# Kernel tuning notes

Measured on AMD Instinct MI355X. Metric: run time of the kernel, lower is better.

## Reference

```python
import jax, jax.numpy as jnp
import numpy as np

DIM = 192
HEADS = 4
CTX = 256
HID = int(DIM * 2.66)  # 510


def _dwconv(x, w):
    # x: (b,c,h,w), w: (c,1,3,3) depthwise
    return jax.lax.conv_general_dilated(
        x, w, window_strides=(1, 1), padding='SAME',
        dimension_numbers=('NCHW', 'OIHW', 'NCHW'),
        feature_group_count=x.shape[1])


def _conv1x1(x, w):
    # w: (out, in)
    return jnp.einsum('oc,bchw->bohw', w, x)


def _layernorm(x, weight, bias):
    # WithBias LayerNorm over channel dim (last dim after to_3d == channels)
    mu = x.mean(axis=1, keepdims=True)
    var = ((x - mu) ** 2).mean(axis=1, keepdims=True)
    xn = (x - mu) / jnp.sqrt(var + 1e-5)
    return xn * weight[None, :, None, None] + bias[None, :, None, None]


def setup_inputs() -> dict:
    key = jax.random.key(0)
    ks = jax.random.split(key, 16)
    s = 0.02
    inp = {
        'x': jax.random.normal(ks[0], (8, DIM, 128, 128), jnp.float32),
        'context_emb': jax.random.normal(ks[1], (8, CTX), jnp.float32),
        'ln1_w': jnp.ones((DIM,), jnp.float32),
        'ln1_b': jnp.zeros((DIM,), jnp.float32),
        'ln2_w': jnp.ones((DIM,), jnp.float32),
        'ln2_b': jnp.zeros((DIM,), jnp.float32),
        'w_qkv': jax.random.normal(ks[2], (3 * DIM, DIM), jnp.float32) * s,
        'w_qkv_dw': jax.random.normal(ks[3], (3 * DIM, 1, 3, 3), jnp.float32) * s,
        'w_proj': jax.random.normal(ks[4], (DIM, DIM), jnp.float32) * s,
        'base_temp': jnp.ones((HEADS, 1, 1), jnp.float32),
        'ta_w1': jax.random.normal(ks[5], (DIM // 4, CTX), jnp.float32) * s,
        'ta_b1': jnp.zeros((DIM // 4,), jnp.float32),
        'ta_w2': jax.random.normal(ks[6], (HEADS, DIM // 4), jnp.float32) * s,
        'ta_b2': jnp.zeros((HEADS,), jnp.float32),
        'vg_w': jax.random.normal(ks[7], (DIM, CTX), jnp.float32) * s,
        'vg_b': jnp.zeros((DIM,), jnp.float32),
        'w_local': jax.random.normal(ks[8], (DIM, 1, 3, 3), jnp.float32) * s,
        'w_ffn_in': jax.random.normal(ks[9], (2 * HID, DIM), jnp.float32) * s,
        'w_ffn_dw': jax.random.normal(ks[10], (2 * HID, 1, 3, 3), jnp.float32) * s,
        'w_ffn_out': jax.random.normal(ks[11], (DIM, HID), jnp.float32) * s,
    }
    return inp


def _forward(x, context_emb, ln1_w, ln1_b, ln2_w, ln2_b, w_qkv, w_qkv_dw,
             w_proj, base_temp, ta_w1, ta_b1, ta_w2, ta_b2, vg_w, vg_b,
             w_local, w_ffn_in, w_ffn_dw, w_ffn_out):
    b, c, h, w = x.shape
    hd = c // HEADS
    scale = hd ** (-0.5)

    # ---- Attention branch ----
    residual = x
    xn = _layernorm(x, ln1_w, ln1_b)

    # context adapters
    t = jax.nn.relu(context_emb @ ta_w1.T + ta_b1) @ ta_w2.T + ta_b2  # (b,heads)
    temp_factor = jax.nn.sigmoid(t)[:, :, None, None] * 2.0 + 0.5    # (b,heads,1,1)
    total_temp = base_temp[None] * temp_factor
    v_gate = jax.nn.sigmoid(context_emb @ vg_w.T + vg_b)             # (b,dim)
    v_gate = v_gate.reshape(b, HEADS, hd, 1)

    qkv = _dwconv(_conv1x1(xn, w_qkv), w_qkv_dw)
    q, k, v = jnp.split(qkv, 3, axis=1)

    def heads_flat(t4):
        return t4.reshape(b, HEADS, hd, h * w)

    qf = heads_flat(q)
    kf = heads_flat(k)
    vf = heads_flat(v)
    qf = qf / jnp.maximum(jnp.linalg.norm(qf, axis=-1, keepdims=True), 1e-12)
    kf = kf / jnp.maximum(jnp.linalg.norm(kf, axis=-1, keepdims=True), 1e-12)

    attn = jnp.einsum('bhcn,bhdn->bhcd', qf, kf) * scale  # (b,heads,hd,hd)
    attn = jax.nn.softmax(attn * total_temp, axis=-1)

    out_global = jnp.einsum('bhcd,bhdn->bhcn', attn, vf * v_gate)
    out_global = out_global.reshape(b, c, h, w)
    out_local = _dwconv(v, w_local)
    x = residual + _conv1x1(out_global + out_local, w_proj)

    # ---- GDFN branch ----
    residual = x
    xn = _layernorm(x, ln2_w, ln2_b)
    y = _dwconv(_conv1x1(xn, w_ffn_in), w_ffn_dw)
    y1, y2 = jnp.split(y, 2, axis=1)
    y = jax.nn.gelu(y1, approximate=False) * y2
    x = residual + _conv1x1(y, w_ffn_out)
    return x


def reference(x, context_emb, ln1_w, ln1_b, ln2_w, ln2_b, w_qkv, w_qkv_dw,
              w_proj, base_temp, ta_w1, ta_b1, ta_w2, ta_b2, vg_w, vg_b,
              w_local, w_ffn_in, w_ffn_dw, w_ffn_out):
    return _forward(x, context_emb, ln1_w, ln1_b, ln2_w, ln2_b, w_qkv,
                    w_qkv_dw, w_proj, base_temp, ta_w1, ta_b1, ta_w2, ta_b2,
                    vg_w, vg_b, w_local, w_ffn_in, w_ffn_dw, w_ffn_out)
```

## Files before the change

### kernel.cpp

```cpp
#include <hip/hip_runtime.h>
#include <math.h>

#define NB 8
#define NC 192
#define NH 128
#define NW 128
#define HW 16384
#define NQ 576
#define NHID 510
#define NHIDP 512
#define NG2 1020
#define NG2P 1024

#define BROWS 32
#define BSLOTS 34
#define BPIX (BSLOTS * NW)
#define BIPIX (BROWS * NW)

typedef unsigned short u16;
typedef short s16x8 __attribute__((ext_vector_type(8)));
typedef float f32x4 __attribute__((ext_vector_type(4)));

#define MFMA_BF16(a, b, c) __builtin_amdgcn_mfma_f32_16x16x32_bf16((a), (b), (c), 0, 0, 0)

__device__ __forceinline__ u16 f2bf(float f) {
  union { float f; unsigned u; } v; v.f = f;
  unsigned r = v.u + 0x7fffu + ((v.u >> 16) & 1u);
  return (u16)(r >> 16);
}
__device__ __forceinline__ float bf2f(u16 h) {
  union { unsigned u; float f; } v; v.u = ((unsigned)h) << 16; return v.f;
}
__device__ __forceinline__ float lo2f(unsigned u) {
  union { unsigned u; float f; } v; v.u = u << 16; return v.f;
}
__device__ __forceinline__ float hi2f(unsigned u) {
  union { unsigned u; float f; } v; v.u = u & 0xffff0000u; return v.f;
}

__global__ void k_prep(const float* __restrict__ wq, const float* __restrict__ wfi,
                       const float* __restrict__ wfo,
                       u16* __restrict__ oq, u16* __restrict__ ofi, u16* __restrict__ ofo) {
  const int n1 = NQ * NC, n2 = NG2P * NC, n3 = NC * NHIDP;
  for (int i = blockIdx.x * blockDim.x + threadIdx.x; i < n1 + n2 + n3;
       i += gridDim.x * blockDim.x) {
    if (i < n1) {
      oq[i] = f2bf(wq[i]);
    } else if (i < n1 + n2) {
      int j = i - n1; int row = j / NC;
      u16 v = 0;
      if (row < NG2) v = f2bf(wfi[j]);
      ofi[j] = v;
    } else {
      int j = i - n1 - n2; int row = j >> 9, col = j & 511;
      u16 v = 0;
      if (col < NHID) v = f2bf(wfo[row * NHID + col]);
      ofo[j] = v;
    }
  }
}

__global__ void k_ctx(const float* __restrict__ ce, const float* __restrict__ taw1,
                      const float* __restrict__ tab1, const float* __restrict__ taw2,
                      const float* __restrict__ tab2, const float* __restrict__ vgw,
                      const float* __restrict__ vgb, const float* __restrict__ btemp,
                      float* __restrict__ tempt, float* __restrict__ vg) {
  int b = blockIdx.x, t = threadIdx.x;
  __shared__ float sce[256];
  __shared__ float shid[48];
  sce[t] = ce[b * 256 + t];
  __syncthreads();
  if (t < 48) {
    float s = tab1[t];
    for (int j = 0; j < 256; j++) s = fmaf(taw1[t * 256 + j], sce[j], s);
    shid[t] = fmaxf(s, 0.f);
  }
  __syncthreads();
  if (t < 4) {
    float s = tab2[t];
    for (int j = 0; j < 48; j++) s = fmaf(taw2[t * 48 + j], shid[j], s);
    float sg = 1.f / (1.f + expf(-s));
    tempt[b * 4 + t] = btemp[t] * (sg * 2.f + 0.5f);
  }
  if (t < 192) {
    float s = vgb[t];
    for (int j = 0; j < 256; j++) s = fmaf(vgw[t * 256 + j], sce[j], s);
    vg[b * 192 + t] = 1.f / (1.f + expf(-s));
  }
}

__global__ __launch_bounds__(256, 2)
void k_ln_gemm_band(const float* __restrict__ in, const float* __restrict__ lnw,
                    const float* __restrict__ lnb, const u16* __restrict__ wbf,
                    u16* __restrict__ out, int nchunks, int row_start, int slot0) {
  __shared__ u16 Xn[64 * 200];
  __shared__ u16 Wc[64 * 200];
  __shared__ float red[512];
  __shared__ float stats[128];
  int t = threadIdx.x;
  int lane = t & 63, wv = t >> 6;
  int bpb = gridDim.x >> 3;
  int b = blockIdx.x / bpb;
  int rb = blockIdx.x - b * bpb;
  int gpx0 = row_start * NW + rb * 64;
  int opx0 = slot0 * NW + rb * 64;
  const float* xp = in + (size_t)b * NC * HW + gpx0 + lane;
  float vals[48];
  float s = 0.f, s2 = 0.f;
#pragma unroll
  for (int j = 0; j < 48; j++) {
    float v = xp[(size_t)(wv * 48 + j) * HW];
    vals[j] = v; s += v; s2 = fmaf(v, v, s2);
  }
  red[wv * 64 + lane] = s;
  red[256 + wv * 64 + lane] = s2;
  __syncthreads();
  if (t < 64) {
    float m = 0.f, q = 0.f;
#pragma unroll
    for (int k = 0; k < 4; k++) { m += red[k * 64 + t]; q += red[256 + k * 64 + t]; }
    m *= (1.f / 192.f);
    float var = q * (1.f / 192.f) - m * m;
    stats[t] = m; stats[64 + t] = rsqrtf(var + 1e-5f);
  }
  __syncthreads();
  float mu = stats[lane], rs = stats[64 + lane];
#pragma unroll
  for (int j = 0; j < 48; j += 2) {
    int c = wv * 48 + j;
    float xa = (vals[j] - mu) * rs * lnw[c] + lnb[c];
    float xb = (vals[j + 1] - mu) * rs * lnw[c + 1] + lnb[c + 1];
    *(unsigned*)&Xn[lane * 200 + c] = (unsigned)f2bf(xa) | ((unsigned)f2bf(xb) << 16);
  }
  int r = lane & 15, grp = lane >> 4;
  int ostride = nchunks << 6;
  for (int nc = 0; nc < nchunks; nc++) {
    __syncthreads();
    for (int i = t; i < 1536; i += 256) {
      int row = i / 24, sg = i % 24;
      *(s16x8*)&Wc[row * 200 + sg * 8] =
          *(const s16x8*)&wbf[(size_t)(nc * 64 + row) * 192 + sg * 8];
    }
    __syncthreads();
    f32x4 z = {0.f, 0.f, 0.f, 0.f};
    f32x4 acc0 = z, acc1 = z, acc2 = z, acc3 = z;
#pragma unroll
    for (int ks = 0; ks < 6; ks++) {
      int k0 = ks * 32 + grp * 8;
      s16x8 a = *(s16x8*)&Xn[(wv * 16 + r) * 200 + k0];
      acc0 = MFMA_BF16(a, *(s16x8*)&Wc[r * 200 + k0], acc0);
      acc1 = MFMA_BF16(a, *(s16x8*)&Wc[(16 + r) * 200 + k0], acc1);
      acc2 = MFMA_BF16(a, *(s16x8*)&Wc[(32 + r) * 200 + k0], acc2);
      acc3 = MFMA_BF16(a, *(s16x8*)&Wc[(48 + r) * 200 + k0], acc3);
    }
    u16* op = out + ((size_t)b * BPIX + opx0 + wv * 16 + grp * 4) * ostride + nc * 64 + r;
#pragma unroll
    for (int i = 0; i < 4; i++) {
      op[(size_t)i * ostride] = f2bf(acc0[i]);
      op[(size_t)i * ostride + 16] = f2bf(acc1[i]);
      op[(size_t)i * ostride + 32] = f2bf(acc2[i]);
      op[(size_t)i * ostride + 48] = f2bf(acc3[i]);
    }
  }
}

__global__ __launch_bounds__(256, 4)
void k_dw_attn_band(const u16* __restrict__ qb_band, const float* __restrict__ wdw,
                    u16* __restrict__ qkb, u16* __restrict__ vpm,
                    float* __restrict__ ssq, int r0) {
  __shared__ u16 Hl[6 * 18 * 64];
  __shared__ float sred[8 * 64];
  int t = threadIdx.x;
  int cc = blockIdx.x % 9;
  int rem = blockIdx.x / 9;
  int b = rem >> 6; int r2 = rem & 63;
  int h0l = (r2 >> 3) * 4, w0 = (r2 & 7) * 16;
  int c0 = cc * 64;
  const s16x8 z8 = {0, 0, 0, 0, 0, 0, 0, 0};
  for (int i = t; i < 864; i += 256) {
    int px = i >> 3, sg = i & 7;
    int hh = px / 18, ww = px % 18;
    int slot = h0l + hh;
    int gh = r0 - 1 + slot;
    int gw = w0 - 1 + ww;
    s16x8 v = z8;
    if (gh >= 0 && gh < NH && gw >= 0 && gw < NW)
      v = *(const s16x8*)&qb_band[((size_t)b * BPIX + slot * NW + gw) * NQ + c0 + sg * 8];
    *(s16x8*)&Hl[(hh * 18 + ww) * 64 + sg * 8] = v;
  }
  __syncthreads();
  int cp = t & 31, psub = t >> 5;
  int pr = psub >> 1, pc0 = (psub & 1) * 8;
  int gc = c0 + 2 * cp;
  float wg0[9], wg1[9];
#pragma unroll
  for (int q = 0; q < 9; q++) { wg0[q] = wdw[gc * 9 + q]; wg1[q] = wdw[(gc + 1) * 9 + q]; }
  bool isv = (c0 >= 384);
  float sq0 = 0.f, sq1 = 0.f;
  s16x8 ov0 = z8, ov1 = z8;
#pragma unroll
  for (int j = 0; j < 8; j++) {
    int pc = pc0 + j;
    float a0 = 0.f, a1 = 0.f;
#pragma unroll
    for (int dr = 0; dr < 3; dr++)
#pragma unroll
      for (int dc = 0; dc < 3; dc++) {
        unsigned u = *(const unsigned*)&Hl[((pr + dr) * 18 + pc + dc) * 64 + 2 * cp];
        a0 = fmaf(lo2f(u), wg0[dr * 3 + dc], a0);
        a1 = fmaf(hi2f(u), wg1[dr * 3 + dc], a1);
      }
    u16 u0 = f2bf(a0), u1 = f2bf(a1);
    if (isv) {
      int gp = (r0 + h0l + pr) * NW + w0 + pc;
      *(unsigned*)&vpm[((size_t)b * HW + gp) * 192 + (gc - 384)] =
          (unsigned)u0 | ((unsigned)u1 << 16);
    } else {
      ov0[j] = (short)u0; ov1[j] = (short)u1;
      float f0 = bf2f(u0), f1 = bf2f(u1);
      sq0 = fmaf(f0, f0, sq0); sq1 = fmaf(f1, f1, sq1);
    }
  }
  if (!isv) {
    int lpx = (h0l + pr) * NW + w0 + pc0;
    *(s16x8*)&qkb[((size_t)b * 384 + gc) * BIPIX + lpx] = ov0;
    *(s16x8*)&qkb[((size_t)b * 384 + gc + 1) * BIPIX + lpx] = ov1;
    sred[psub * 64 + 2 * cp] = sq0;
    sred[psub * 64 + 2 * cp + 1] = sq1;
    __syncthreads();
    if (t < 64) {
      float sa = 0.f;
#pragma unroll
      for (int p8 = 0; p8 < 8; p8++) sa += sred[p8 * 64 + t];
      atomicAdd(&ssq[b * 384 + c0 + t], sa);
    }
  }
}

__global__ __launch_bounds__(256, 2)
void k_attn_band(const u16* __restrict__ qkb, float* __restrict__ attn) {
  __shared__ float par[4 * 2304];
  int t = threadIdx.x;
  int lane = t & 63, wv = t >> 6;
  int r = lane & 15, grp = lane >> 4;
  int bh = blockIdx.x >> 2, kc = blockIdx.x & 3;
  int b = bh >> 2, h = bh & 3;
  const u16* qb = qkb + ((size_t)b * 384 + h * 48) * BIPIX;
  const u16* kb = qkb + ((size_t)b * 384 + 192 + h * 48) * BIPIX;
  f32x4 z = {0.f, 0.f, 0.f, 0.f};
  f32x4 acc[3][3];
#pragma unroll
  for (int i = 0; i < 3; i++)
#pragma unroll
    for (int j = 0; j < 3; j++) acc[i][j] = z;
  int kbase = kc * 1024 + wv * 256 + grp * 8;
#pragma unroll 2
  for (int ks = 0; ks < 8; ks++) {
    int k0 = kbase + ks * 32;
    s16x8 af[3], bf[3];
#pragma unroll
    for (int mt = 0; mt < 3; mt++) af[mt] = *(const s16x8*)&qb[(size_t)(mt * 16 + r) * BIPIX + k0];
#pragma unroll
    for (int nt = 0; nt < 3; nt++) bf[nt] = *(const s16x8*)&kb[(size_t)(nt * 16 + r) * BIPIX + k0];
#pragma unroll
    for (int mt = 0; mt < 3; mt++)
#pragma unroll
      for (int nt = 0; nt < 3; nt++) acc[mt][nt] = MFMA_BF16(af[mt], bf[nt], acc[mt][nt]);
  }
#pragma unroll
  for (int mt = 0; mt < 3; mt++)
#pragma unroll
    for (int nt = 0; nt < 3; nt++)
#pragma unroll
      for (int i = 0; i < 4; i++)
        par[wv * 2304 + (mt * 16 + grp * 4 + i) * 48 + nt * 16 + r] = acc[mt][nt][i];
  __syncthreads();
  float* ag = attn + (size_t)bh * 2304;
  for (int i = t; i < 2304; i += 256)
    atomicAdd(&ag[i], par[i] + par[2304 + i] + par[4608 + i] + par[6912 + i]);
}

__global__ void k_softmax(float* __restrict__ attn, const float* __restrict__ ssq,
                          const float* __restrict__ tempt, const float* __restrict__ vg) {
  int bh = blockIdx.x, b = bh >> 2, h = bh & 3;
  int t = threadIdx.x;
  __shared__ float srk[48], svg[48];
  if (t < 48) {
    float nk = sqrtf(ssq[b * 384 + 192 + h * 48 + t]);
    srk[t] = 1.f / fmaxf(nk, 1e-12f);
    svg[t] = vg[b * 192 + h * 48 + t];
  }
  __syncthreads();
  if (t < 48) {
    float nq = sqrtf(ssq[b * 384 + h * 48 + t]);
    float rq = 1.f / fmaxf(nq, 1e-12f);
    float sc = 0.14433756729740643f * tempt[b * 4 + h] * rq;
    float* row = attn + (size_t)bh * 2304 + t * 48;
    float l[48]; float mx = -1e30f;
#pragma unroll
    for (int d = 0; d < 48; d++) { l[d] = row[d] * srk[d] * sc; mx = fmaxf(mx, l[d]); }
    float ss = 0.f;
#pragma unroll
    for (int d = 0; d < 48; d++) { l[d] = expf(l[d] - mx); ss += l[d]; }
    float inv = 1.f / ss;
#pragma unroll
    for (int d = 0; d < 48; d++) row[d] = l[d] * inv * svg[d];
  }
}

__global__ __launch_bounds__(256)
void k_wd(const float* __restrict__ attn, const float* __restrict__ wp,
          u16* __restrict__ wdg) {
  __shared__ float am[4 * 48 * 48];
  int b = blockIdx.x >> 3, oc = blockIdx.x & 7;
  int t = threadIdx.x;
  const float* ag = attn + (size_t)b * 4 * 2304;
  for (int i = t; i < 9216; i += 256) am[i] = ag[i];
  __syncthreads();
  u16* wdb = wdg + (size_t)b * 192 * 384;
  for (int idx = t; idx < 24 * 384; idx += 256) {
    int oo = idx / 384, j = idx % 384;
    int o = oc * 24 + oo;
    float val;
    if (j < 192) {
      int hj = j / 48, dj = j % 48;
      const float* wpo = wp + o * 192 + hj * 48;
      const float* ap = am + hj * 2304 + dj;
      float sa = 0.f;
#pragma unroll
      for (int c = 0; c < 48; c++) sa = fmaf(wpo[c], ap[c * 48], sa);
      val = sa;
    } else {
      val = wp[o * 192 + (j - 192)];
    }
    wdb[o * 384 + j] = f2bf(val);
  }
}

__global__ __launch_bounds__(256, 2)
void k_proj(const u16* __restrict__ vpm, const float* __restrict__ wl,
            const u16* __restrict__ wdg, const float* __restrict__ x,
            float* __restrict__ x2) {
  __shared__ u16 Hl[6 * 18 * 64];
  __shared__ u16 Xl[64 * 392];
  int t = threadIdx.x;
  int b = blockIdx.x >> 8; int r2 = blockIdx.x & 255;
  int h0 = (r2 >> 3) * 4, w0 = (r2 & 7) * 16;
  int cp = t & 31, psub = t >> 5;
  int pr = psub >> 1, pc0 = (psub & 1) * 8;
  const s16x8 z8 = {0, 0, 0, 0, 0, 0, 0, 0};
  for (int c3 = 0; c3 < 3; c3++) {
    int c0 = c3 * 64;
    __syncthreads();
    for (int i = t; i < 864; i += 256) {
      int px = i >> 3, sg = i & 7;
      int hh = px / 18, ww = px % 18;
      int gh = h0 - 1 + hh, gw = w0 - 1 + ww;
      s16x8 v = z8;
      if (gh >= 0 && gh < NH && gw >= 0 && gw < NW)
        v = *(const s16x8*)&vpm[((size_t)b * HW + gh * NW + gw) * 192 + c0 + sg * 8];
      *(s16x8*)&Hl[(hh * 18 + ww) * 64 + sg * 8] = v;
    }
    __syncthreads();
    int gc = c0 + 2 * cp;
    float wg0[9], wg1[9];
#pragma unroll
    for (int q = 0; q < 9; q++) { wg0[q] = wl[gc * 9 + q]; wg1[q] = wl[(gc + 1) * 9 + q]; }
#pragma unroll
    for (int j = 0; j < 8; j++) {
      int pc = pc0 + j; int p = pr * 16 + pc;
      float a0 = 0.f, a1 = 0.f; unsigned uc = 0;
#pragma unroll
      for (int dr = 0; dr < 3; dr++)
#pragma unroll
        for (int dc = 0; dc < 3; dc++) {
          unsigned u = *(const unsigned*)&Hl[((pr + dr) * 18 + pc + dc) * 64 + 2 * cp];
          if (dr == 1 && dc == 1) uc = u;
          a0 = fmaf(lo2f(u), wg0[dr * 3 + dc], a0);
          a1 = fmaf(hi2f(u), wg1[dr * 3 + dc], a1);
        }
      *(unsigned*)&Xl[p * 392 + gc] = uc;
      *(unsigned*)&Xl[p * 392 + 192 + gc] =
          (unsigned)f2bf(a0) | ((unsigned)f2bf(a1) << 16);
    }
  }
  __syncthreads();
  int lane = t & 63, wv = t >> 6;
  int r = lane & 15, grp = lane >> 4;
  const u16* wdb = wdg + (size_t)b * 192 * 384;
  f32x4 z = {0.f, 0.f, 0.f, 0.f};
  f32x4 acc[3][4];
#pragma unroll
  for (int i = 0; i < 3; i++)
#pragma unroll
    for (int j = 0; j < 4; j++) acc[i][j] = z;
#pragma unroll 2
  for (int ks = 0; ks < 12; ks++) {
    int k0 = ks * 32 + grp * 8;
    s16x8 b0 = *(s16x8*)&Xl[r * 392 + k0];
    s16x8 b1 = *(s16x8*)&Xl[(16 + r) * 392 + k0];
    s16x8 b2 = *(s16x8*)&Xl[(32 + r) * 392 + k0];
    s16x8 b3 = *(s16x8*)&Xl[(48 + r) * 392 + k0];
#pragma unroll
    for (int mt = 0; mt < 3; mt++) {
      s16x8 a = *(const s16x8*)&wdb[(size_t)(wv * 48 + mt * 16 + r) * 384 + k0];
      acc[mt][0] = MFMA_BF16(a, b0, acc[mt][0]);
      acc[mt][1] = MFMA_BF16(a, b1, acc[mt][1]);
      acc[mt][2] = MFMA_BF16(a, b2, acc[mt][2]);
      acc[mt][3] = MFMA_BF16(a, b3, acc[mt][3]);
    }
  }
#pragma unroll
  for (int mt = 0; mt < 3; mt++)
#pragma unroll
    for (int nt = 0; nt < 4; nt++) {
      size_t base = ((size_t)b * NC + wv * 48 + mt * 16 + grp * 4) * HW +
                    (h0 + nt) * NW + w0 + r;
#pragma unroll
      for (int i = 0; i < 4; i++) {
        size_t idx = base + (size_t)i * HW;
        x2[idx] = acc[mt][nt][i] + x[idx];
      }
    }
}

__global__ __launch_bounds__(256, 2)
void k_gelu_band(const u16* __restrict__ ypre, const float* __restrict__ wdwf,
                 u16* __restrict__ ypm, int r0) {
  __shared__ u16 H1[6 * 18 * 64];
  __shared__ u16 H2[6 * 18 * 72];
  int t = threadIdx.x;
  int jc = blockIdx.x & 7; int rem = blockIdx.x >> 3;
  int b = rem >> 6; int r2 = rem & 63;
  int h0l = (r2 >> 3) * 4, w0 = (r2 & 7) * 16;
  int j0 = jc * 64;
  int base2 = j0 + 504;
  const s16x8 z8 = {0, 0, 0, 0, 0, 0, 0, 0};
  for (int i = t; i < 864; i += 256) {
    int px = i >> 3, sg = i & 7;
    int hh = px / 18, ww = px % 18;
    int slot = h0l + hh;
    int gh = r0 - 1 + slot, gw = w0 - 1 + ww;
    s16x8 v = z8;
    if (gh >= 0 && gh < NH && gw >= 0 && gw < NW)
      v = *(const s16x8*)&ypre[((size_t)b * BPIX + slot * NW + gw) * NG2P + j0 + sg * 8];
    *(s16x8*)&H1[(hh * 18 + ww) * 64 + sg * 8] = v;
  }
  for (int i = t; i < 972; i += 256) {
    int px = i / 9, sg = i % 9;
    int hh = px / 18, ww = px % 18;
    int slot = h0l + hh;
    int gh = r0 - 1 + slot, gw = w0 - 1 + ww;
    s16x8 v = z8;
    if (gh >= 0 && gh < NH && gw >= 0 && gw < NW)
      v = *(const s16x8*)&ypre[((size_t)b * BPIX + slot * NW + gw) * NG2P + base2 + sg * 8];
    *(s16x8*)&H2[(hh * 18 + ww) * 72 + sg * 8] = v;
  }
  __syncthreads();
  int cp = t & 31, psub = t >> 5;
  int pr = psub >> 1, pc0 = (psub & 1) * 8;
  int jl = 2 * cp; int j = j0 + jl;
  bool v0 = (j < NHID), v1 = (j + 1 < NHID);
  float w1a[9], w1b[9], w2a[9], w2b[9];
#pragma unroll
  for (int q = 0; q < 9; q++) {
    w1a[q] = 0.f; w1b[q] = 0.f; w2a[q] = 0.f; w2b[q] = 0.f;
    if (v0) { w1a[q] = wdwf[j * 9 + q]; w2a[q] = wdwf[(j + NHID) * 9 + q]; }
    if (v1) { w1b[q] = wdwf[(j + 1) * 9 + q]; w2b[q] = wdwf[(j + 1 + NHID) * 9 + q]; }
  }
#pragma unroll
  for (int jj = 0; jj < 8; jj++) {
    int pc = pc0 + jj;
    float d1a = 0.f, d1b = 0.f, d2a = 0.f, d2b = 0.f;
#pragma unroll
    for (int dr = 0; dr < 3; dr++)
#pragma unroll
      for (int dc = 0; dc < 3; dc++) {
        int q = dr * 3 + dc;
        unsigned u1 = *(const unsigned*)&H1[((pr + dr) * 18 + pc + dc) * 64 + jl];
        unsigned u2 = *(const unsigned*)&H2[((pr + dr) * 18 + pc + dc) * 72 + jl + 6];
        d1a = fmaf(lo2f(u1), w1a[q], d1a); d1b = fmaf(hi2f(u1), w1b[q], d1b);
        d2a = fmaf(lo2f(u2), w2a[q], d2a); d2b = fmaf(hi2f(u2), w2b[q], d2b);
      }
    float ga = 0.5f * d1a * (1.f + erff(d1a * 0.70710678118654752f));
    float gb = 0.5f * d1b * (1.f + erff(d1b * 0.70710678118654752f));
    float ya = v0 ? ga * d2a : 0.f;
    float yb = v1 ? gb * d2b : 0.f;
    int lpx = (h0l + pr) * NW + w0 + pc;
    *(unsigned*)&ypm[((size_t)b * BIPIX + lpx) * NHIDP + j] =
        (unsigned)f2bf(ya) | ((unsigned)f2bf(yb) << 16);
  }
}

__global__ __launch_bounds__(256, 2)
void k_ffnout_band(const u16* __restrict__ ypm, const u16* __restrict__ wfo,
                   const float* __restrict__ x2, float* __restrict__ out, int r0) {
  __shared__ u16 Yt[64 * 520];
  int t = threadIdx.x;
  int b = blockIdx.x >> 6; int px0l = (blockIdx.x & 63) << 6;
  for (int i = t; i < 4096; i += 256) {
    int row = i >> 6, sg = i & 63;
    *(s16x8*)&Yt[row * 520 + sg * 8] =
        *(const s16x8*)&ypm[((size_t)b * BIPIX + px0l + row) * NHIDP + sg * 8];
  }
  __syncthreads();
  int lane = t & 63, wv = t >> 6;
  int r = lane & 15, grp = lane >> 4;
  f32x4 z = {0.f, 0.f, 0.f, 0.f};
  f32x4 acc[3][4];
#pragma unroll
  for (int i = 0; i < 3; i++)
#pragma unroll
    for (int j = 0; j < 4; j++) acc[i][j] = z;
#pragma unroll 2
  for (int ks = 0; ks < 16; ks++) {
    int k0 = ks * 32 + grp * 8;
    s16x8 b0 = *(s16x8*)&Yt[r * 520 + k0];
    s16x8 b1 = *(s16x8*)&Yt[(16 + r) * 520 + k0];
    s16x8 b2 = *(s16x8*)&Yt[(32 + r) * 520 + k0];
    s16x8 b3 = *(s16x8*)&Yt[(48 + r) * 520 + k0];
#pragma unroll
    for (int mt = 0; mt < 3; mt++) {
      s16x8 a = *(const s16x8*)&wfo[(size_t)(wv * 48 + mt * 16 + r) * NHIDP + k0];
      acc[mt][0] = MFMA_BF16(a, b0, acc[mt][0]);
      acc[mt][1] = MFMA_BF16(a, b1, acc[mt][1]);
      acc[mt][2] = MFMA_BF16(a, b2, acc[mt][2]);
      acc[mt][3] = MFMA_BF16(a, b3, acc[mt][3]);
    }
  }
  int gpx0 = r0 * NW + px0l;
#pragma unroll
  for (int mt = 0; mt < 3; mt++)
#pragma unroll
    for (int nt = 0; nt < 4; nt++) {
      size_t base = ((size_t)b * NC + wv * 48 + mt * 16 + grp * 4) * HW + gpx0 + nt * 16 + r;
#pragma unroll
      for (int i = 0; i < 4; i++) {
        size_t idx = base + (size_t)i * HW;
        out[idx] = acc[mt][nt][i] + x2[idx];
      }
    }
}

extern "C" void kernel_launch(void* const* d_in, const int* in_sizes, int n_in,
                              void* d_out, int out_size, void* d_ws, size_t ws_size,
                              hipStream_t stream) {
  const float* x      = (const float*)d_in[0];
  const float* ce     = (const float*)d_in[1];
  const float* ln1w   = (const float*)d_in[2];
  const float* ln1b   = (const float*)d_in[3];
  const float* ln2w   = (const float*)d_in[4];
  const float* ln2b   = (const float*)d_in[5];
  const float* wqkv   = (const float*)d_in[6];
  const float* wqkvdw = (const float*)d_in[7];
  const float* wproj  = (const float*)d_in[8];
  const float* btemp  = (const float*)d_in[9];
  const float* taw1   = (const float*)d_in[10];
  const float* tab1   = (const float*)d_in[11];
  const float* taw2   = (const float*)d_in[12];
  const float* tab2   = (const float*)d_in[13];
  const float* vgw    = (const float*)d_in[14];
  const float* vgb    = (const float*)d_in[15];
  const float* wlocal = (const float*)d_in[16];
  const float* wffni  = (const float*)d_in[17];
  const float* wffndw = (const float*)d_in[18];
  const float* wffno  = (const float*)d_in[19];
  float* outp = (float*)d_out;
  char* ws = (char*)d_ws;

  const size_t REQUIRED = 224602240ULL;
  if (ws_size < REQUIRED) {
    hipMemsetAsync(d_out, 0, (size_t)out_size * 4, stream);
    return;
  }
  u16*   wq_bf   = (u16*)(ws + 0);
  u16*   wfi_bf  = (u16*)(ws + 221184);
  u16*   wfo_bf  = (u16*)(ws + 614400);
  float* tempt   = (float*)(ws + 811008);
  float* vg      = (float*)(ws + 811136);
  float* ssq     = (float*)(ws + 817280);
  float* attn    = (float*)(ws + 829568);
  u16*   wdg     = (u16*)(ws + 1124480);
  u16*   qkvband = (u16*)(ws + 2304128);
  u16*   qkband  = (u16*)(ws + 42412160);
  u16*   ypreband= (u16*)(ws + 2304128);
  u16*   vpm     = (u16*)(ws + 73607296);
  u16*   ypmband = (u16*)(ws + 73607296);
  float* x2      = (float*)(ws + 123938944);

  hipMemsetAsync(ws + 817280, 0, 12288 + 294912, stream);
  k_prep<<<512, 256, 0, stream>>>(wqkv, wffni, wffno, wq_bf, wfi_bf, wfo_bf);
  k_ctx<<<8, 256, 0, stream>>>(ce, taw1, tab1, taw2, tab2, vgw, vgb, btemp, tempt, vg);

  for (int band = 0; band < 4; band++) {
    int r0 = band * BROWS;
    int rs = (r0 > 0) ? r0 - 1 : 0;
    int re = (r0 + BROWS + 1 < NH) ? r0 + BROWS + 1 : NH;
    int nr = re - rs;
    int s0 = rs - (r0 - 1);
    k_ln_gemm_band<<<8 * nr * 2, 256, 0, stream>>>(x, ln1w, ln1b, wq_bf, qkvband, 9, rs, s0);
    k_dw_attn_band<<<9 * 8 * 64, 256, 0, stream>>>(qkvband, wqkvdw, qkband, vpm, ssq, r0);
    k_attn_band<<<32 * 4, 256, 0, stream>>>(qkband, attn);
  }
  k_softmax<<<32, 64, 0, stream>>>(attn, ssq, tempt, vg);
  k_wd<<<64, 256, 0, stream>>>(attn, wproj, wdg);
  k_proj<<<2048, 256, 0, stream>>>(vpm, wlocal, wdg, x, x2);

  for (int band = 0; band < 4; band++) {
    int r0 = band * BROWS;
    int rs = (r0 > 0) ? r0 - 1 : 0;
    int re = (r0 + BROWS + 1 < NH) ? r0 + BROWS + 1 : NH;
    int nr = re - rs;
    int s0 = rs - (r0 - 1);
    k_ln_gemm_band<<<8 * nr * 2, 256, 0, stream>>>(x2, ln2w, ln2b, wfi_bf, ypreband, 16, rs, s0);
    k_gelu_band<<<8 * 8 * 64, 256, 0, stream>>>(ypreband, wffndw, ypmband, r0);
    k_ffnout_band<<<8 * 64, 256, 0, stream>>>(ypmband, wfo_bf, x2, outp, r0);
  }
}
```

Baseline: 1.241 ms.

## Widen proj/ffnout GEMMs to 8 waves with register prefetch; split attn K further

k_proj and k_ffnout_band move to 512-thread blocks. Eight waves now split the 64-pixel tile into two halves, and each wave computes a 48x32 output instead of 48x64. Those two kernels also gain software prefetching of the next K-slice of A and B fragments into registers, and their launch bounds are raised to (512,4). k_attn_band splits the reduction dimension into 8 chunks instead of 4, doubling the grid to get more parallelism. The tighter launch bounds cap the register budget and could cause spills, and the extra K chunks add more partial-sum reduction work.

```diff
diff --git a/kernel.cpp b/kernel.cpp
--- a/kernel.cpp
+++ b/kernel.cpp
@@ -243,7 +243,7 @@
   int t = threadIdx.x;
   int lane = t & 63, wv = t >> 6;
   int r = lane & 15, grp = lane >> 4;
-  int bh = blockIdx.x >> 2, kc = blockIdx.x & 3;
+  int bh = blockIdx.x >> 3, kc = blockIdx.x & 7;
   int b = bh >> 2, h = bh & 3;
   const u16* qb = qkb + ((size_t)b * 384 + h * 48) * BIPIX;
   const u16* kb = qkb + ((size_t)b * 384 + 192 + h * 48) * BIPIX;
@@ -253,9 +253,9 @@
   for (int i = 0; i < 3; i++)
 #pragma unroll
     for (int j = 0; j < 3; j++) acc[i][j] = z;
-  int kbase = kc * 1024 + wv * 256 + grp * 8;
-#pragma unroll 2
-  for (int ks = 0; ks < 8; ks++) {
+  int kbase = kc * 512 + wv * 128 + grp * 8;
+#pragma unroll
+  for (int ks = 0; ks < 4; ks++) {
     int k0 = kbase + ks * 32;
     s16x8 af[3], bf[3];
 #pragma unroll
@@ -337,7 +337,7 @@
   }
 }
 
-__global__ __launch_bounds__(256, 2)
+__global__ __launch_bounds__(512, 4)
 void k_proj(const u16* __restrict__ vpm, const float* __restrict__ wl,
             const u16* __restrict__ wdg, const float* __restrict__ x,
             float* __restrict__ x2) {
@@ -345,14 +345,15 @@
   __shared__ u16 Xl[64 * 392];
   int t = threadIdx.x;
   int b = blockIdx.x >> 8; int r2 = blockIdx.x & 255;
-  int h0 = (r2 >> 3) * 4, w0 = (r2 & 7) * 16;
+  int h0 = (r2 >> 3) * 4, w0 = (r2 & 8 - 1) * 16;
+  w0 = (r2 & 7) * 16;
   int cp = t & 31, psub = t >> 5;
-  int pr = psub >> 1, pc0 = (psub & 1) * 8;
+  int pr = psub >> 2, pc0 = (psub & 3) * 4;
   const s16x8 z8 = {0, 0, 0, 0, 0, 0, 0, 0};
   for (int c3 = 0; c3 < 3; c3++) {
     int c0 = c3 * 64;
     __syncthreads();
-    for (int i = t; i < 864; i += 256) {
+    for (int i = t; i < 864; i += 512) {
       int px = i >> 3, sg = i & 7;
       int hh = px / 18, ww = px % 18;
       int gh = h0 - 1 + hh, gw = w0 - 1 + ww;
@@ -367,7 +368,7 @@
 #pragma unroll
     for (int q = 0; q < 9; q++) { wg0[q] = wl[gc * 9 + q]; wg1[q] = wl[(gc + 1) * 9 + q]; }
 #pragma unroll
-    for (int j = 0; j < 8; j++) {
+    for (int j = 0; j < 4; j++) {
       int pc = pc0 + j; int p = pr * 16 + pc;
       float a0 = 0.f, a1 = 0.f; unsigned uc = 0;
 #pragma unroll
@@ -387,35 +388,48 @@
   __syncthreads();
   int lane = t & 63, wv = t >> 6;
   int r = lane & 15, grp = lane >> 4;
+  int wvc = wv & 3, wvp = wv >> 2;
   const u16* wdb = wdg + (size_t)b * 192 * 384;
+  const u16* ar0 = wdb + (size_t)(wvc * 48 + r) * 384 + grp * 8;
+  const u16* ar1 = ar0 + 16 * 384;
+  const u16* ar2 = ar0 + 32 * 384;
+  const u16* xb0 = &Xl[(wvp * 32 + r) * 392 + grp * 8];
+  const u16* xb1 = xb0 + 16 * 392;
   f32x4 z = {0.f, 0.f, 0.f, 0.f};
-  f32x4 acc[3][4];
+  f32x4 acc[3][2];
 #pragma unroll
   for (int i = 0; i < 3; i++)
 #pragma unroll
-    for (int j = 0; j < 4; j++) acc[i][j] = z;
+    for (int j = 0; j < 2; j++) acc[i][j] = z;
+  s16x8 a0 = *(const s16x8*)ar0;
+  s16x8 a1 = *(const s16x8*)ar1;
+  s16x8 a2 = *(const s16x8*)ar2;
+  s16x8 b0 = *(const s16x8*)xb0;
+  s16x8 b1 = *(const s16x8*)xb1;
 #pragma unroll 2
   for (int ks = 0; ks < 12; ks++) {
-    int k0 = ks * 32 + grp * 8;
-    s16x8 b0 = *(s16x8*)&Xl[r * 392 + k0];
-    s16x8 b1 = *(s16x8*)&Xl[(16 + r) * 392 + k0];
-    s16x8 b2 = *(s16x8*)&Xl[(32 + r) * 392 + k0];
-    s16x8 b3 = *(s16x8*)&Xl[(48 + r) * 392 + k0];
-#pragma unroll
-    for (int mt = 0; mt < 3; mt++) {
-      s16x8 a = *(const s16x8*)&wdb[(size_t)(wv * 48 + mt * 16 + r) * 384 + k0];
-      acc[mt][0] = MFMA_BF16(a, b0, acc[mt][0]);
-      acc[mt][1] = MFMA_BF16(a, b1, acc[mt][1]);
-      acc[mt][2] = MFMA_BF16(a, b2, acc[mt][2]);
-      acc[mt][3] = MFMA_BF16(a, b3, acc[mt][3]);
-    }
+    s16x8 ca0 = a0, ca1 = a1, ca2 = a2, cb0 = b0, cb1 = b1;
+    if (ks < 11) {
+      int off = (ks + 1) * 32;
+      a0 = *(const s16x8*)(ar0 + off);
+      a1 = *(const s16x8*)(ar1 + off);
+      a2 = *(const s16x8*)(ar2 + off);
+      b0 = *(const s16x8*)(xb0 + off);
+      b1 = *(const s16x8*)(xb1 + off);
+    }
+    acc[0][0] = MFMA_BF16(ca0, cb0, acc[0][0]);
+    acc[0][1] = MFMA_BF16(ca0, cb1, acc[0][1]);
+    acc[1][0] = MFMA_BF16(ca1, cb0, acc[1][0]);
+    acc[1][1] = MFMA_BF16(ca1, cb1, acc[1][1]);
+    acc[2][0] = MFMA_BF16(ca2, cb0, acc[2][0]);
+    acc[2][1] = MFMA_BF16(ca2, cb1, acc[2][1]);
   }
 #pragma unroll
   for (int mt = 0; mt < 3; mt++)
 #pragma unroll
-    for (int nt = 0; nt < 4; nt++) {
-      size_t base = ((size_t)b * NC + wv * 48 + mt * 16 + grp * 4) * HW +
-                    (h0 + nt) * NW + w0 + r;
+    for (int nt = 0; nt < 2; nt++) {
+      size_t base = ((size_t)b * NC + wvc * 48 + mt * 16 + grp * 4) * HW +
+                    (h0 + wvp * 2 + nt) * NW + w0 + r;
 #pragma unroll
       for (int i = 0; i < 4; i++) {
         size_t idx = base + (size_t)i * HW;
@@ -492,13 +506,13 @@
   }
 }
 
-__global__ __launch_bounds__(256, 2)
+__global__ __launch_bounds__(512, 4)
 void k_ffnout_band(const u16* __restrict__ ypm, const u16* __restrict__ wfo,
                    const float* __restrict__ x2, float* __restrict__ out, int r0) {
   __shared__ u16 Yt[64 * 520];
   int t = threadIdx.x;
   int b = blockIdx.x >> 6; int px0l = (blockIdx.x & 63) << 6;
-  for (int i = t; i < 4096; i += 256) {
+  for (int i = t; i < 4096; i += 512) {
     int row = i >> 6, sg = i & 63;
     *(s16x8*)&Yt[row * 520 + sg * 8] =
         *(const s16x8*)&ypm[((size_t)b * BIPIX + px0l + row) * NHIDP + sg * 8];
@@ -506,34 +520,48 @@
   __syncthreads();
   int lane = t & 63, wv = t >> 6;
   int r = lane & 15, grp = lane >> 4;
+  int wvc = wv & 3, wvp = wv >> 2;
+  const u16* ar0 = wfo + (size_t)(wvc * 48 + r) * NHIDP + grp * 8;
+  const u16* ar1 = ar0 + 16 * NHIDP;
+  const u16* ar2 = ar0 + 32 * NHIDP;
+  const u16* yb0 = &Yt[(wvp * 32 + r) * 520 + grp * 8];
+  const u16* yb1 = yb0 + 16 * 520;
   f32x4 z = {0.f, 0.f, 0.f, 0.f};
-  f32x4 acc[3][4];
+  f32x4 acc[3][2];
 #pragma unroll
   for (int i = 0; i < 3; i++)
 #pragma unroll
-    for (int j = 0; j < 4; j++) acc[i][j] = z;
+    for (int j = 0; j < 2; j++) acc[i][j] = z;
+  s16x8 a0 = *(const s16x8*)ar0;
+  s16x8 a1 = *(const s16x8*)ar1;
+  s16x8 a2 = *(const s16x8*)ar2;
+  s16x8 b0 = *(const s16x8*)yb0;
+  s16x8 b1 = *(const s16x8*)yb1;
 #pragma unroll 2
   for (int ks = 0; ks < 16; ks++) {
-    int k0 = ks * 32 + grp * 8;
-    s16x8 b0 = *(s16x8*)&Yt[r * 520 + k0];
-    s16x8 b1 = *(s16x8*)&Yt[(16 + r) * 520 + k0];
-    s16x8 b2 = *(s16x8*)&Yt[(32 + r) * 520 + k0];
-    s16x8 b3 = *(s16x8*)&Yt[(48 + r) * 520 + k0];
-#pragma unroll
-    for (int mt = 0; mt < 3; mt++) {
-      s16x8 a = *(const s16x8*)&wfo[(size_t)(wv * 48 + mt * 16 + r) * NHIDP + k0];
-      acc[mt][0] = MFMA_BF16(a, b0, acc[mt][0]);
-      acc[mt][1] = MFMA_BF16(a, b1, acc[mt][1]);
-      acc[mt][2] = MFMA_BF16(a, b2, acc[mt][2]);
-      acc[mt][3] = MFMA_BF16(a, b3, acc[mt][3]);
-    }
+    s16x8 ca0 = a0, ca1 = a1, ca2 = a2, cb0 = b0, cb1 = b1;
+    if (ks < 15) {
+      int off = (ks + 1) * 32;
+      a0 = *(const s16x8*)(ar0 + off);
+      a1 = *(const s16x8*)(ar1 + off);
+      a2 = *(const s16x8*)(ar2 + off);
+      b0 = *(const s16x8*)(yb0 + off);
+      b1 = *(const s16x8*)(yb1 + off);
+    }
+    acc[0][0] = MFMA_BF16(ca0, cb0, acc[0][0]);
+    acc[0][1] = MFMA_BF16(ca0, cb1, acc[0][1]);
+    acc[1][0] = MFMA_BF16(ca1, cb0, acc[1][0]);
+    acc[1][1] = MFMA_BF16(ca1, cb1, acc[1][1]);
+    acc[2][0] = MFMA_BF16(ca2, cb0, acc[2][0]);
+    acc[2][1] = MFMA_BF16(ca2, cb1, acc[2][1]);
   }
   int gpx0 = r0 * NW + px0l;
 #pragma unroll
   for (int mt = 0; mt < 3; mt++)
 #pragma unroll
-    for (int nt = 0; nt < 4; nt++) {
-      size_t base = ((size_t)b * NC + wv * 48 + mt * 16 + grp * 4) * HW + gpx0 + nt * 16 + r;
+    for (int nt = 0; nt < 2; nt++) {
+      size_t base = ((size_t)b * NC + wvc * 48 + mt * 16 + grp * 4) * HW +
+                    gpx0 + wvp * 32 + nt * 16 + r;
 #pragma unroll
       for (int i = 0; i < 4; i++) {
         size_t idx = base + (size_t)i * HW;
@@ -600,11 +628,11 @@
     int s0 = rs - (r0 - 1);
     k_ln_gemm_band<<<8 * nr * 2, 256, 0, stream>>>(x, ln1w, ln1b, wq_bf, qkvband, 9, rs, s0);
     k_dw_attn_band<<<9 * 8 * 64, 256, 0, stream>>>(qkvband, wqkvdw, qkband, vpm, ssq, r0);
-    k_attn_band<<<32 * 4, 256, 0, stream>>>(qkband, attn);
+    k_attn_band<<<32 * 8, 256, 0, stream>>>(qkband, attn);
   }
   k_softmax<<<32, 64, 0, stream>>>(attn, ssq, tempt, vg);
   k_wd<<<64, 256, 0, stream>>>(attn, wproj, wdg);
-  k_proj<<<2048, 256, 0, stream>>>(vpm, wlocal, wdg, x, x2);
+  k_proj<<<2048, 512, 0, stream>>>(vpm, wlocal, wdg, x, x2);
 
   for (int band = 0; band < 4; band++) {
     int r0 = band * BROWS;
@@ -614,6 +642,6 @@
     int s0 = rs - (r0 - 1);
     k_ln_gemm_band<<<8 * nr * 2, 256, 0, stream>>>(x2, ln2w, ln2b, wfi_bf, ypreband, 16, rs, s0);
     k_gelu_band<<<8 * 8 * 64, 256, 0, stream>>>(ypreband, wffndw, ypmband, r0);
-    k_ffnout_band<<<8 * 64, 256, 0, stream>>>(ypmband, wfo_bf, x2, outp, r0);
-  }
-}
+    k_ffnout_band<<<8 * 64, 512, 0, stream>>>(ypmband, wfo_bf, x2, outp, r0);
+  }
+}
```

New measurement: 1.256 ms. No clear change (+1.2%).

## Fuse depthwise-conv GELU gating with FFN output projection per tile

Applied to the files above, without the earlier changes.

Merges the GELU-gated depthwise conv kernel and the FFN output GEMM into one kernel. Each block loops over the eight 64-channel hidden chunks, writes the gated activations for its 4x16 pixel tile into a small shared buffer, and accumulates the output projection with MFMA right away. This avoids writing and re-reading the bf16 hidden intermediate in global memory and drops one launch per band. In exchange the grid shrinks eightfold to 512 blocks, which do serial chunk loops with extra barriers, so there is less parallelism to hide latency.

```diff
diff --git a/kernel.cpp b/kernel.cpp
--- a/kernel.cpp
+++ b/kernel.cpp
@@ -425,115 +425,107 @@
 }
 
 __global__ __launch_bounds__(256, 2)
-void k_gelu_band(const u16* __restrict__ ypre, const float* __restrict__ wdwf,
-                 u16* __restrict__ ypm, int r0) {
+void k_gelu_ffn_band(const u16* __restrict__ ypre, const float* __restrict__ wdwf,
+                     const u16* __restrict__ wfo, const float* __restrict__ x2,
+                     float* __restrict__ out, int r0) {
   __shared__ u16 H1[6 * 18 * 64];
   __shared__ u16 H2[6 * 18 * 72];
+  __shared__ u16 Yc[64 * 80];
   int t = threadIdx.x;
-  int jc = blockIdx.x & 7; int rem = blockIdx.x >> 3;
-  int b = rem >> 6; int r2 = rem & 63;
+  int b = blockIdx.x >> 6; int r2 = blockIdx.x & 63;
   int h0l = (r2 >> 3) * 4, w0 = (r2 & 7) * 16;
-  int j0 = jc * 64;
-  int base2 = j0 + 504;
-  const s16x8 z8 = {0, 0, 0, 0, 0, 0, 0, 0};
-  for (int i = t; i < 864; i += 256) {
-    int px = i >> 3, sg = i & 7;
-    int hh = px / 18, ww = px % 18;
-    int slot = h0l + hh;
-    int gh = r0 - 1 + slot, gw = w0 - 1 + ww;
-    s16x8 v = z8;
-    if (gh >= 0 && gh < NH && gw >= 0 && gw < NW)
-      v = *(const s16x8*)&ypre[((size_t)b * BPIX + slot * NW + gw) * NG2P + j0 + sg * 8];
-    *(s16x8*)&H1[(hh * 18 + ww) * 64 + sg * 8] = v;
-  }
-  for (int i = t; i < 972; i += 256) {
-    int px = i / 9, sg = i % 9;
-    int hh = px / 18, ww = px % 18;
-    int slot = h0l + hh;
-    int gh = r0 - 1 + slot, gw = w0 - 1 + ww;
-    s16x8 v = z8;
-    if (gh >= 0 && gh < NH && gw >= 0 && gw < NW)
-      v = *(const s16x8*)&ypre[((size_t)b * BPIX + slot * NW + gw) * NG2P + base2 + sg * 8];
-    *(s16x8*)&H2[(hh * 18 + ww) * 72 + sg * 8] = v;
-  }
-  __syncthreads();
   int cp = t & 31, psub = t >> 5;
   int pr = psub >> 1, pc0 = (psub & 1) * 8;
-  int jl = 2 * cp; int j = j0 + jl;
-  bool v0 = (j < NHID), v1 = (j + 1 < NHID);
-  float w1a[9], w1b[9], w2a[9], w2b[9];
-#pragma unroll
-  for (int q = 0; q < 9; q++) {
-    w1a[q] = 0.f; w1b[q] = 0.f; w2a[q] = 0.f; w2b[q] = 0.f;
-    if (v0) { w1a[q] = wdwf[j * 9 + q]; w2a[q] = wdwf[(j + NHID) * 9 + q]; }
-    if (v1) { w1b[q] = wdwf[(j + 1) * 9 + q]; w2b[q] = wdwf[(j + 1 + NHID) * 9 + q]; }
-  }
-#pragma unroll
-  for (int jj = 0; jj < 8; jj++) {
-    int pc = pc0 + jj;
-    float d1a = 0.f, d1b = 0.f, d2a = 0.f, d2b = 0.f;
-#pragma unroll
-    for (int dr = 0; dr < 3; dr++)
-#pragma unroll
-      for (int dc = 0; dc < 3; dc++) {
-        int q = dr * 3 + dc;
-        unsigned u1 = *(const unsigned*)&H1[((pr + dr) * 18 + pc + dc) * 64 + jl];
-        unsigned u2 = *(const unsigned*)&H2[((pr + dr) * 18 + pc + dc) * 72 + jl + 6];
-        d1a = fmaf(lo2f(u1), w1a[q], d1a); d1b = fmaf(hi2f(u1), w1b[q], d1b);
-        d2a = fmaf(lo2f(u2), w2a[q], d2a); d2b = fmaf(hi2f(u2), w2b[q], d2b);
-      }
-    float ga = 0.5f * d1a * (1.f + erff(d1a * 0.70710678118654752f));
-    float gb = 0.5f * d1b * (1.f + erff(d1b * 0.70710678118654752f));
-    float ya = v0 ? ga * d2a : 0.f;
-    float yb = v1 ? gb * d2b : 0.f;
-    int lpx = (h0l + pr) * NW + w0 + pc;
-    *(unsigned*)&ypm[((size_t)b * BIPIX + lpx) * NHIDP + j] =
-        (unsigned)f2bf(ya) | ((unsigned)f2bf(yb) << 16);
-  }
-}
-
-__global__ __launch_bounds__(256, 2)
-void k_ffnout_band(const u16* __restrict__ ypm, const u16* __restrict__ wfo,
-                   const float* __restrict__ x2, float* __restrict__ out, int r0) {
-  __shared__ u16 Yt[64 * 520];
-  int t = threadIdx.x;
-  int b = blockIdx.x >> 6; int px0l = (blockIdx.x & 63) << 6;
-  for (int i = t; i < 4096; i += 256) {
-    int row = i >> 6, sg = i & 63;
-    *(s16x8*)&Yt[row * 520 + sg * 8] =
-        *(const s16x8*)&ypm[((size_t)b * BIPIX + px0l + row) * NHIDP + sg * 8];
-  }
-  __syncthreads();
   int lane = t & 63, wv = t >> 6;
   int r = lane & 15, grp = lane >> 4;
+  int jl = 2 * cp;
+  const s16x8 z8 = {0, 0, 0, 0, 0, 0, 0, 0};
   f32x4 z = {0.f, 0.f, 0.f, 0.f};
   f32x4 acc[3][4];
 #pragma unroll
   for (int i = 0; i < 3; i++)
 #pragma unroll
     for (int j = 0; j < 4; j++) acc[i][j] = z;
-#pragma unroll 2
-  for (int ks = 0; ks < 16; ks++) {
-    int k0 = ks * 32 + grp * 8;
-    s16x8 b0 = *(s16x8*)&Yt[r * 520 + k0];
-    s16x8 b1 = *(s16x8*)&Yt[(16 + r) * 520 + k0];
-    s16x8 b2 = *(s16x8*)&Yt[(32 + r) * 520 + k0];
-    s16x8 b3 = *(s16x8*)&Yt[(48 + r) * 520 + k0];
-#pragma unroll
-    for (int mt = 0; mt < 3; mt++) {
-      s16x8 a = *(const s16x8*)&wfo[(size_t)(wv * 48 + mt * 16 + r) * NHIDP + k0];
-      acc[mt][0] = MFMA_BF16(a, b0, acc[mt][0]);
-      acc[mt][1] = MFMA_BF16(a, b1, acc[mt][1]);
-      acc[mt][2] = MFMA_BF16(a, b2, acc[mt][2]);
-      acc[mt][3] = MFMA_BF16(a, b3, acc[mt][3]);
-    }
-  }
-  int gpx0 = r0 * NW + px0l;
+
+  for (int jc = 0; jc < 8; jc++) {
+    int j0 = jc * 64;
+    int base2 = j0 + 504;
+    __syncthreads();
+    for (int i = t; i < 864; i += 256) {
+      int px = i >> 3, sg = i & 7;
+      int hh = px / 18, ww = px % 18;
+      int slot = h0l + hh;
+      int gh = r0 - 1 + slot, gw = w0 - 1 + ww;
+      s16x8 v = z8;
+      if (gh >= 0 && gh < NH && gw >= 0 && gw < NW)
+        v = *(const s16x8*)&ypre[((size_t)b * BPIX + slot * NW + gw) * NG2P + j0 + sg * 8];
+      *(s16x8*)&H1[(hh * 18 + ww) * 64 + sg * 8] = v;
+    }
+    for (int i = t; i < 972; i += 256) {
+      int px = i / 9, sg = i % 9;
+      int hh = px / 18, ww = px % 18;
+      int slot = h0l + hh;
+      int gh = r0 - 1 + slot, gw = w0 - 1 + ww;
+      s16x8 v = z8;
+      if (gh >= 0 && gh < NH && gw >= 0 && gw < NW)
+        v = *(const s16x8*)&ypre[((size_t)b * BPIX + slot * NW + gw) * NG2P + base2 + sg * 8];
+      *(s16x8*)&H2[(hh * 18 + ww) * 72 + sg * 8] = v;
+    }
+    __syncthreads();
+    int j = j0 + jl;
+    bool v0 = (j < NHID), v1 = (j + 1 < NHID);
+    float w1a[9], w1b[9], w2a[9], w2b[9];
+#pragma unroll
+    for (int q = 0; q < 9; q++) {
+      w1a[q] = 0.f; w1b[q] = 0.f; w2a[q] = 0.f; w2b[q] = 0.f;
+      if (v0) { w1a[q] = wdwf[j * 9 + q]; w2a[q] = wdwf[(j + NHID) * 9 + q]; }
+      if (v1) { w1b[q] = wdwf[(j + 1) * 9 + q]; w2b[q] = wdwf[(j + 1 + NHID) * 9 + q]; }
+    }
+#pragma unroll
+    for (int jj = 0; jj < 8; jj++) {
+      int pc = pc0 + jj;
+      float d1a = 0.f, d1b = 0.f, d2a = 0.f, d2b = 0.f;
+#pragma unroll
+      for (int dr = 0; dr < 3; dr++)
+#pragma unroll
+        for (int dc = 0; dc < 3; dc++) {
+          int q = dr * 3 + dc;
+          unsigned u1 = *(const unsigned*)&H1[((pr + dr) * 18 + pc + dc) * 64 + jl];
+          unsigned u2 = *(const unsigned*)&H2[((pr + dr) * 18 + pc + dc) * 72 + jl + 6];
+          d1a = fmaf(lo2f(u1), w1a[q], d1a); d1b = fmaf(hi2f(u1), w1b[q], d1b);
+          d2a = fmaf(lo2f(u2), w2a[q], d2a); d2b = fmaf(hi2f(u2), w2b[q], d2b);
+        }
+      float ga = 0.5f * d1a * (1.f + erff(d1a * 0.70710678118654752f));
+      float gb = 0.5f * d1b * (1.f + erff(d1b * 0.70710678118654752f));
+      float ya = v0 ? ga * d2a : 0.f;
+      float yb = v1 ? gb * d2b : 0.f;
+      int lp = pr * 16 + pc;
+      *(unsigned*)&Yc[lp * 80 + jl] = (unsigned)f2bf(ya) | ((unsigned)f2bf(yb) << 16);
+    }
+    __syncthreads();
+#pragma unroll
+    for (int ks = 0; ks < 2; ks++) {
+      int k0 = ks * 32 + grp * 8;
+      s16x8 b0 = *(s16x8*)&Yc[r * 80 + k0];
+      s16x8 b1 = *(s16x8*)&Yc[(16 + r) * 80 + k0];
+      s16x8 b2 = *(s16x8*)&Yc[(32 + r) * 80 + k0];
+      s16x8 b3 = *(s16x8*)&Yc[(48 + r) * 80 + k0];
+#pragma unroll
+      for (int mt = 0; mt < 3; mt++) {
+        s16x8 a = *(const s16x8*)&wfo[(size_t)(wv * 48 + mt * 16 + r) * NHIDP + j0 + k0];
+        acc[mt][0] = MFMA_BF16(a, b0, acc[mt][0]);
+        acc[mt][1] = MFMA_BF16(a, b1, acc[mt][1]);
+        acc[mt][2] = MFMA_BF16(a, b2, acc[mt][2]);
+        acc[mt][3] = MFMA_BF16(a, b3, acc[mt][3]);
+      }
+    }
+  }
 #pragma unroll
   for (int mt = 0; mt < 3; mt++)
 #pragma unroll
     for (int nt = 0; nt < 4; nt++) {
-      size_t base = ((size_t)b * NC + wv * 48 + mt * 16 + grp * 4) * HW + gpx0 + nt * 16 + r;
+      size_t base = ((size_t)b * NC + wv * 48 + mt * 16 + grp * 4) * HW +
+                    (r0 + h0l + nt) * NW + w0 + r;
 #pragma unroll
       for (int i = 0; i < 4; i++) {
         size_t idx = base + (size_t)i * HW;
@@ -585,7 +577,6 @@
   u16*   qkband  = (u16*)(ws + 42412160);
   u16*   ypreband= (u16*)(ws + 2304128);
   u16*   vpm     = (u16*)(ws + 73607296);
-  u16*   ypmband = (u16*)(ws + 73607296);
   float* x2      = (float*)(ws + 123938944);
 
   hipMemsetAsync(ws + 817280, 0, 12288 + 294912, stream);
@@ -613,7 +604,6 @@
     int nr = re - rs;
     int s0 = rs - (r0 - 1);
     k_ln_gemm_band<<<8 * nr * 2, 256, 0, stream>>>(x2, ln2w, ln2b, wfi_bf, ypreband, 16, rs, s0);
-    k_gelu_band<<<8 * 8 * 64, 256, 0, stream>>>(ypreband, wffndw, ypmband, r0);
-    k_ffnout_band<<<8 * 64, 256, 0, stream>>>(ypmband, wfo_bf, x2, outp, r0);
-  }
-}
+    k_gelu_ffn_band<<<8 * 64, 256, 0, stream>>>(ypreband, wffndw, wfo_bf, x2, outp, r0);
+  }
+}
```

Result: faster. 1.211 ms (-2.4%).
